# Performance work log

Hardware: AMD Instinct MI355X
Metric: run time of the kernel (lower is better)

Reference implementation:

```python
import jax, jax.numpy as jnp
import numpy as np

IN_CH = 8      # in_channels
CIN = 80       # cin_channels (mel)
DI_BASE = 2
POS_GROUP = 4
NCH = 256      # n_channels
NLAYERS = 8
K = 3          # kernel_size
B = 1          # spect batch; audio batch = B * POS_GROUP
T = 4096
C2L = 2 * NCH * NLAYERS


def _conv1x1(x, w, b):
    # x: [B, C, T], w: [O, C], b: [O]
    return jnp.einsum('bct,oc->bot', x, w) + b[None, :, None]


def _dilated_conv(x, w, b, dilation):
    # x: [B, C, T], w: [O, C, K], 'same' padding as in torch Conv1d
    pad = dilation * (K - 1) // 2
    y = jax.lax.conv_general_dilated(
        x, w, window_strides=(1,), padding=[(pad, pad)],
        rhs_dilation=(dilation,), dimension_numbers=('NCH', 'OIH', 'NCH'))
    return y + b[None, :, None]


def setup_inputs() -> dict:
    key = jax.random.key(0)
    ks = jax.random.split(key, 12)
    s = 0.05
    d = {}
    d['audio'] = jax.random.normal(ks[0], (B * POS_GROUP, IN_CH, T), jnp.float32)
    d['spect'] = jax.random.normal(ks[1], (B, CIN, T), jnp.float32)
    d['pos'] = jax.random.randint(ks[2], (B * POS_GROUP,), 0, POS_GROUP)
    d['start_w'] = jax.random.normal(ks[3], (NCH, IN_CH), jnp.float32) * s
    d['start_b'] = jnp.zeros((NCH,), jnp.float32)
    d['cond_w'] = jax.random.normal(ks[4], (C2L, CIN), jnp.float32) * s
    d['cond_b'] = jnp.zeros((C2L,), jnp.float32)
    d['pos_emb_w'] = jax.random.normal(ks[5], (POS_GROUP, 128), jnp.float32) * s
    d['pos_lin_w'] = jax.random.normal(ks[6], (C2L, 128), jnp.float32) * s
    d['pos_lin_b'] = jnp.zeros((C2L,), jnp.float32)
    d['in_w'] = jax.random.normal(ks[7], (NLAYERS, 2 * NCH, NCH, K), jnp.float32) * s
    d['in_b'] = jnp.zeros((NLAYERS, 2 * NCH), jnp.float32)
    d['rs_w'] = jax.random.normal(ks[8], (NLAYERS - 1, 2 * NCH, NCH), jnp.float32) * s
    d['rs_b'] = jnp.zeros((NLAYERS - 1, 2 * NCH), jnp.float32)
    d['rs_last_w'] = jax.random.normal(ks[9], (NCH, NCH), jnp.float32) * s
    d['rs_last_b'] = jnp.zeros((NCH,), jnp.float32)
    d['end_w'] = jax.random.normal(ks[10], (2 * IN_CH, NCH), jnp.float32) * s
    d['end_b'] = jnp.zeros((2 * IN_CH,), jnp.float32)
    return d


def reference(audio, spect, pos, start_w, start_b, cond_w, cond_b,
              pos_emb_w, pos_lin_w, pos_lin_b, in_w, in_b,
              rs_w, rs_b, rs_last_w, rs_last_b, end_w, end_b):
    h = _conv1x1(audio, start_w, start_b)               # [BG, NCH, T]
    out = jnp.zeros_like(h)
    cond = _conv1x1(spect, cond_w, cond_b)              # [B, 2*NCH*L, T]
    # repeat(1, pos_group, 1).view(-1, C, T) == consecutive batch tiling
    cond = jnp.repeat(cond, POS_GROUP, axis=0)          # [BG, 2*NCH*L, T]
    pe = jax.nn.relu(pos_emb_w[pos])                    # [BG, 128]
    pc = (pe @ pos_lin_w.T + pos_lin_b)[:, :, None]     # [BG, 2*NCH*L, 1]
    for i in range(NLAYERS):
        off = i * 2 * NCH
        in_act = (_dilated_conv(h, in_w[i], in_b[i], DI_BASE ** i)
                  + cond[:, off:off + 2 * NCH]
                  + pc[:, off:off + 2 * NCH])
        acts = jnp.tanh(in_act[:, :NCH]) * jax.nn.sigmoid(in_act[:, NCH:])
        if i < NLAYERS - 1:
            rs = _conv1x1(acts, rs_w[i], rs_b[i])       # [BG, 2*NCH, T]
            h = h + rs[:, :NCH]
            out = out + rs[:, NCH:]
        else:
            out = out + _conv1x1(acts, rs_last_w, rs_last_b)
    y = _conv1x1(out, end_w, end_b)                     # [BG, 2*IN_CH, T]
    return y[:, :IN_CH], y[:, IN_CH:]
```

## Files before the change

### kernel.cpp

```cpp
#include <hip/hip_runtime.h>
#include <stdint.h>

#define T_LEN 4096
#define PAD   128
#define HROWS (T_LEN + 2*PAD)
#define NCH   256
#define M2    512
#define BG    4
#define NL    8

using f4  = __attribute__((ext_vector_type(4))) float;
using bh8 = __attribute__((ext_vector_type(8))) short;
using s4v = __attribute__((ext_vector_type(4))) short;
using u4  = __attribute__((ext_vector_type(4))) unsigned int;

static __device__ __forceinline__ short f2b(float f){
  unsigned u = __builtin_bit_cast(unsigned, f);
  unsigned r = (u + 0x7FFFu + ((u >> 16) & 1u)) >> 16;
  return (short)r;
}
static __device__ __forceinline__ float b2f(short s){
  unsigned u = ((unsigned)(unsigned short)s) << 16;
  return __builtin_bit_cast(float, u);
}

#define MFMA(a,b,c) __builtin_amdgcn_mfma_f32_16x16x32_bf16((a),(b),(c),0,0,0)

#define W_BLK0   0
#define PAD_BLK0 1024
#define E_BLK0   1280
#define ST_BLK0  1408
#define CB_BLK0  1536
#define H0_BLK0  1600
#define ALL_BLKS 1856

__global__ __launch_bounds__(256) void prep_all(
    const float* __restrict__ audio, const float* __restrict__ spect,
    const int* __restrict__ pos, const float* __restrict__ start_w,
    const float* __restrict__ start_b, const float* __restrict__ cond_w,
    const float* __restrict__ pos_emb_w, const float* __restrict__ pos_lin_w,
    const float* __restrict__ pos_lin_b, const float* __restrict__ in_w,
    const float* __restrict__ in_b, const float* __restrict__ rs_w,
    const float* __restrict__ rs_b, const float* __restrict__ rs_last_w,
    const float* __restrict__ rs_last_b, const float* __restrict__ end_w,
    const float* __restrict__ end_b,
    short* __restrict__ W1, short* __restrict__ W2, float* __restrict__ rsb8,
    short* __restrict__ Wc, short* __restrict__ hA, short* __restrict__ hB,
    short* __restrict__ Es, float* __restrict__ ebl, short* __restrict__ spectT,
    float* __restrict__ cb){
  __shared__ float smem[4224];
  const int bid = blockIdx.x, tid = threadIdx.x;

  if (bid < PAD_BLK0){
    const int n1 = NL*3*M2*NCH, n2 = NL*4*8*4*64*8, n3 = NL*M2, n4 = 4096*128;
    for (int i = bid*256 + tid; i < n1+n2+n3+n4; i += 1024*256){
      if (i < n1){
        int j = i & 7, lane = (i >> 3) & 63, mf = (i >> 9) & 3, kk = (i >> 11) & 7, og = (i >> 14) & 7;
        int lt = i >> 17;
        int tap = lt % 3, l = lt / 3;
        int o = og*64 + mf*16 + (lane & 15);
        int c = kk*32 + (lane >> 4)*8 + j;
        W1[i] = f2b(in_w[(((l*M2 + o)*NCH + c)*3) + tap]);
      } else if (i < n1+n2){
        int q = i - n1;
        int j = q & 7, lane = (q >> 3) & 63, mf = (q >> 9) & 3, kk = (q >> 11) & 7, og = (q >> 14) & 3;
        int l = q >> 16;
        int o = og*64 + mf*16 + (lane & 15);
        int c = kk*32 + (lane >> 4)*8 + j;
        W2[q] = (l < 7) ? f2b(rs_w[((size_t)(l*M2 + o))*NCH + c]) : (short)0;
      } else if (i < n1+n2+n3){
        int k = i - n1 - n2;
        int o = k & 511, l = k >> 9;
        rsb8[k] = (l < 7) ? rs_b[l*M2 + o] : 0.f;
      } else {
        int j = i - n1 - n2 - n3;
        int k = j & 127, o = j >> 7;
        Wc[j] = (k < 80) ? f2b(cond_w[o*80 + k]) : (short)0;
      }
    }
  } else if (bid < E_BLK0){
    int i = (bid - PAD_BLK0)*256 + tid;
    short* h = (i < 32768) ? hA : hB;
    int j = (i & 32767) << 3;
    int b = j >> 16;
    int r = j & 65535;
    int row = r >> 8, c = r & 255;
    int grow = (row < PAD) ? row : (T_LEN + PAD + (row - PAD));
    *(u4*)(h + ((size_t)b*HROWS + grow)*NCH + c) = (u4){0,0,0,0};
  } else if (bid < ST_BLK0){
    float* ew_s = smem; float* red = smem + 256;
    int e = bid - E_BLK0;
    const int l = e >> 4, o = e & 15;
    const int c = tid;
    ew_s[c] = end_w[o*256 + c];
    __syncthreads();
    const float* Wsrc = (l < 7) ? (rs_w + ((size_t)(l*M2 + NCH))*NCH) : rs_last_w;
    float acc = 0.f;
    #pragma unroll 8
    for (int cp = 0; cp < 256; ++cp)
      acc += ew_s[cp] * Wsrc[(size_t)cp*NCH + c];
    int kk = c >> 5, g = (c >> 3) & 3, j = c & 7;
    Es[(((size_t)l*8 + kk)*64 + g*16 + o)*8 + j] = f2b(acc);
    float bv = (l < 7) ? rs_b[l*M2 + NCH + c] : rs_last_b[c];
    red[c] = ew_s[c] * bv;
    __syncthreads();
    for (int s = 128; s > 0; s >>= 1){
      if (c < s) red[c] += red[c + s];
      __syncthreads();
    }
    if (c == 0) ebl[l*16 + o] = red[0] + ((l == 0) ? end_b[o] : 0.f);
  } else if (bid < CB_BLK0){
    float (*tile)[65] = (float(*)[65])smem;
    int e = bid - ST_BLK0;
    int t0 = (e & 63)*64, k0 = (e >> 6)*64;
    for (int i = tid; i < 64*64; i += 256){
      int kr = i >> 6, tt = i & 63;
      int k = k0 + kr;
      tile[kr][tt] = (k < 80) ? spect[(size_t)k*T_LEN + t0 + tt] : 0.f;
    }
    __syncthreads();
    for (int i = tid; i < 64*64; i += 256){
      int r = i >> 6, kk = i & 63;
      spectT[(size_t)(t0 + r)*128 + k0 + kk] = f2b(tile[kk][r]);
    }
  } else if (bid < H0_BLK0){
    int e = bid - CB_BLK0;
    int b = e >> 4;
    int ch = (e & 15)*256 + tid;
    int p = pos[b];
    float acc = pos_lin_b[ch] + in_b[ch];
    for (int k = 0; k < 128; ++k){
      float ev = pos_emb_w[p*128 + k];
      ev = ev > 0.f ? ev : 0.f;
      acc += ev * pos_lin_w[ch*128 + k];
    }
    cb[b*4096 + ch] = acc;
  } else {
    float* sw = smem; float* sb = smem + 2048;
    int e = bid - H0_BLK0;
    int b = e >> 6, t0 = (e & 63)*64;
    for (int i = tid; i < NCH*8; i += 256) sw[i] = start_w[i];
    for (int i = tid; i < NCH;   i += 256) sb[i] = start_b[i];
    __syncthreads();
    int t = t0 + (tid & 63);
    int cg = tid >> 6;
    float av[8];
    #pragma unroll
    for (int ic = 0; ic < 8; ++ic) av[ic] = audio[((size_t)(b*8 + ic))*T_LEN + t];
    short* dst = hA + ((size_t)b*HROWS + PAD + t)*NCH;
    for (int c = cg*64; c < cg*64 + 64; ++c){
      float acc = sb[c];
      #pragma unroll
      for (int ic = 0; ic < 8; ++ic) acc += sw[c*8 + ic]*av[ic];
      dst[c] = f2b(acc);
    }
  }
}

__global__ __launch_bounds__(512, 2) void cond_gemm(
    const short* __restrict__ Wc, const short* __restrict__ spectT,
    const float* __restrict__ cond_b, short* __restrict__ cond){
  __shared__ short St[64*128];
  const int tid = threadIdx.x;
  const int w = tid >> 6, lane = tid & 63;
  const int l15 = lane & 15, g = lane >> 4;
  const int t0 = blockIdx.x*64, ch0 = blockIdx.y*512;
  const int orow = w << 6;

  #pragma unroll
  for (int s = 0; s < 2; ++s){
    int id = tid + s*512;
    int r = id >> 4, c8 = (id & 15) << 3;
    u4 v = *(const u4*)(spectT + (size_t)(t0 + r)*128 + c8);
    *(u4*)(St + r*128 + (c8 ^ ((r & 7) << 3))) = v;
  }
  __syncthreads();

  f4 acc[4][4];
  #pragma unroll
  for (int mf = 0; mf < 4; ++mf)
    #pragma unroll
    for (int nf = 0; nf < 4; ++nf) acc[mf][nf] = (f4){0.f,0.f,0.f,0.f};

  #pragma unroll
  for (int kk = 0; kk < 3; ++kk){
    bh8 av[4], bv[4];
    #pragma unroll
    for (int mf = 0; mf < 4; ++mf)
      av[mf] = *(const bh8*)(Wc + (size_t)(ch0 + orow + mf*16 + l15)*128 + kk*32 + g*8);
    #pragma unroll
    for (int nf = 0; nf < 4; ++nf){
      int t = nf*16 + l15;
      bv[nf] = *(const bh8*)(St + t*128 + ((kk*32 + g*8) ^ ((t & 7) << 3)));
    }
    #pragma unroll
    for (int mf = 0; mf < 4; ++mf)
      #pragma unroll
      for (int nf = 0; nf < 4; ++nf)
        acc[mf][nf] = MFMA(av[mf], bv[nf], acc[mf][nf]);
  }

  short* cbase = cond + (((size_t)(blockIdx.y*64 + blockIdx.x)*8 + w)*16)*256 + lane*4;
  #pragma unroll
  for (int mf = 0; mf < 4; ++mf){
    f4 bb = *(const f4*)(cond_b + ch0 + orow + mf*16 + 4*g);
    #pragma unroll
    for (int nf = 0; nf < 4; ++nf){
      s4v pk;
      #pragma unroll
      for (int j = 0; j < 4; ++j) pk[j] = f2b(acc[mf][nf][j] + bb[j]);
      *(s4v*)(cbase + (mf*4 + nf)*256) = pk;
    }
  }
}

__global__ __launch_bounds__(512, 2) void wn_layer(
    const short* __restrict__ hSrc, short* __restrict__ hDst,
    const short* __restrict__ W1l, const short* __restrict__ W2l,
    const short* __restrict__ Esl, const short* __restrict__ condl,
    const float* __restrict__ cb_l, const float* __restrict__ rsb_l,
    const float* __restrict__ ebl_l, float* __restrict__ yacc,
    int dil, int flags){

  __shared__ short Ht[3*64*NCH];
  __shared__ short xb[64*NCH];

  const int tid  = threadIdx.x;
  const int w    = tid >> 6, lane = tid & 63;
  const int l15  = lane & 15, g = lane >> 4;
  const int tile = blockIdx.x, b = blockIdx.y;
  const int orow = w << 6;
  const int sw8  = (l15 & 7) << 3;
  const bool first = flags & 1, last = flags & 2;

  f4 acc[4][4];
  #pragma unroll
  for (int mf = 0; mf < 4; ++mf)
    #pragma unroll
    for (int nf = 0; nf < 4; ++nf) acc[mf][nf] = (f4){0.f,0.f,0.f,0.f};

  bh8 Ap[3][4], Bp[3][4];

#define LA1(S, BUF) do{ const int _tap=(S)>>3, _kk=(S)&7; \
    const short* _p = W1l + (_tap<<17) + (w<<14) + (_kk<<11) + lane*8; \
    Ap[BUF][0]=*(const bh8*)(_p);      Ap[BUF][1]=*(const bh8*)(_p+512); \
    Ap[BUF][2]=*(const bh8*)(_p+1024); Ap[BUF][3]=*(const bh8*)(_p+1536); }while(0)
#define LB1(S, BUF) do{ const int _tap=(S)>>3, _kk=(S)&7; const int _c=(_kk*32+g*8)^sw8; \
    Bp[BUF][0]=*(const bh8*)(Ht + _tap*16384 + ( 0+l15)*NCH + _c); \
    Bp[BUF][1]=*(const bh8*)(Ht + _tap*16384 + (16+l15)*NCH + _c); \
    Bp[BUF][2]=*(const bh8*)(Ht + _tap*16384 + (32+l15)*NCH + _c); \
    Bp[BUF][3]=*(const bh8*)(Ht + _tap*16384 + (48+l15)*NCH + _c); }while(0)
#define LA2(S, BUF) do{ const int _kk=(S); \
    const short* _p = W2l + (w<<14) + (_kk<<11) + lane*8; \
    Ap[BUF][0]=*(const bh8*)(_p);      Ap[BUF][1]=*(const bh8*)(_p+512); \
    Ap[BUF][2]=*(const bh8*)(_p+1024); Ap[BUF][3]=*(const bh8*)(_p+1536); }while(0)
#define LB2(S, BUF) do{ const int _c=((S)*32+g*8)^sw8; \
    Bp[BUF][0]=*(const bh8*)(xb + ( 0+l15)*NCH + _c); \
    Bp[BUF][1]=*(const bh8*)(xb + (16+l15)*NCH + _c); \
    Bp[BUF][2]=*(const bh8*)(xb + (32+l15)*NCH + _c); \
    Bp[BUF][3]=*(const bh8*)(xb + (48+l15)*NCH + _c); }while(0)

  LA1(0, 0);

  {
    const int rsub = tid >> 5;
    const int innr = (tid & 31) << 3;
    #pragma unroll
    for (int tap = 0; tap < 3; ++tap){
      const int gbase = b*HROWS + PAD + tile*64 + (tap-1)*dil;
      #pragma unroll
      for (int ch = 0; ch < 4; ++ch){
        int r = ch*16 + rsub;
        u4 v = *(const u4*)(hSrc + (size_t)(gbase + r)*NCH + innr);
        *(u4*)(Ht + tap*16384 + r*NCH + (innr ^ ((r & 7) << 3))) = v;
      }
    }
  }
  s4v cvf[4][4];
  {
    const short* cbase = condl + (((size_t)tile*8 + w)*16)*256 + lane*4;
    #pragma unroll
    for (int mf = 0; mf < 4; ++mf)
      #pragma unroll
      for (int nf = 0; nf < 4; ++nf)
        cvf[mf][nf] = *(const s4v*)(cbase + (mf*4 + nf)*256);
  }
  __syncthreads();

  LB1(0, 0);
  LA1(1, 1); LB1(1, 1);
  #pragma unroll
  for (int s = 0; s < 24; ++s){
    const int cur = s % 3, pf = (s+2) % 3;
    if (s < 22){ LA1(s+2, pf); LB1(s+2, pf); }
    #pragma unroll
    for (int mf = 0; mf < 4; ++mf)
      #pragma unroll
      for (int nf = 0; nf < 4; ++nf)
        acc[mf][nf] = MFMA(Ap[cur][mf], Bp[cur][nf], acc[mf][nf]);
  }

  float bias[4][4];
  #pragma unroll
  for (int mf = 0; mf < 4; ++mf){
    f4 t = *(const f4*)(cb_l + b*4096 + orow + mf*16 + 4*g);
    #pragma unroll
    for (int j = 0; j < 4; ++j) bias[mf][j] = t[j];
  }
  float rbv[4][4];
  #pragma unroll
  for (int mf = 0; mf < 4; ++mf){
    f4 t = *(const f4*)(rsb_l + orow + mf*16 + 4*g);
    #pragma unroll
    for (int j = 0; j < 4; ++j) rbv[mf][j] = t[j];
  }

  if (w >= 4){
    #pragma unroll
    for (int mf = 0; mf < 4; ++mf){
      #pragma unroll
      for (int nf = 0; nf < 4; ++nf){
        int tl = nf*16 + l15;
        s4v pk;
        #pragma unroll
        for (int j = 0; j < 4; ++j){
          float x = acc[mf][nf][j] + bias[mf][j] + b2f(cvf[mf][nf][j]);
          x = fminf(fmaxf(x, -30.f), 30.f);
          pk[j] = f2b(1.f/(1.f + __expf(-x)));
        }
        int cb0 = (orow - NCH) + mf*16 + 4*g;
        *(s4v*)(xb + tl*NCH + (cb0 ^ sw8)) = pk;
      }
    }
  }
  __syncthreads();
  if (w < 4){
    #pragma unroll
    for (int mf = 0; mf < 4; ++mf){
      #pragma unroll
      for (int nf = 0; nf < 4; ++nf){
        int tl = nf*16 + l15;
        int cb0 = orow + mf*16 + 4*g;
        short* p = xb + tl*NCH + (cb0 ^ sw8);
        s4v sg = *(const s4v*)p;
        s4v pk;
        #pragma unroll
        for (int j = 0; j < 4; ++j){
          float x = acc[mf][nf][j] + bias[mf][j] + b2f(cvf[mf][nf][j]);
          x = fminf(fmaxf(x, -30.f), 30.f);
          float e = __expf(2.f*x);
          float th = (e - 1.f)/(e + 1.f);
          pk[j] = f2b(th * b2f(sg[j]));
        }
        *(s4v*)p = pk;
      }
    }
    if (!last) LA2(0, 0);
  }
  __syncthreads();

  if (w < 4){
    if (!last){
      #pragma unroll
      for (int mf = 0; mf < 4; ++mf)
        #pragma unroll
        for (int nf = 0; nf < 4; ++nf) acc[mf][nf] = (f4){0.f,0.f,0.f,0.f};
      LB2(0, 0);
      #pragma unroll
      for (int s = 0; s < 8; ++s){
        const int cur = s & 1, nxt = cur ^ 1;
        if (s < 7){ LA2(s+1, nxt); LB2(s+1, nxt); }
        #pragma unroll
        for (int mf = 0; mf < 4; ++mf)
          #pragma unroll
          for (int nf = 0; nf < 4; ++nf)
            acc[mf][nf] = MFMA(Ap[cur][mf], Bp[cur][nf], acc[mf][nf]);
      }
      #pragma unroll
      for (int mf = 0; mf < 4; ++mf){
        #pragma unroll
        for (int nf = 0; nf < 4; ++nf){
          int tl = nf*16 + l15;
          int cb0 = orow + mf*16 + 4*g;
          s4v hold = *(const s4v*)(Ht + 16384 + tl*NCH + (cb0 ^ sw8));
          s4v pk;
          #pragma unroll
          for (int j = 0; j < 4; ++j)
            pk[j] = f2b(b2f(hold[j]) + acc[mf][nf][j] + rbv[mf][j]);
          *(s4v*)(hDst + ((size_t)b*HROWS + PAD + tile*64 + tl)*NCH + cb0) = pk;
        }
      }
    }
  } else {
    const int q = w - 4;
    f4 ya = (f4){0.f,0.f,0.f,0.f};
    #pragma unroll
    for (int kk = 0; kk < 8; ++kk){
      bh8 av = *(const bh8*)(Esl + ((size_t)kk*64 + lane)*8);
      int _c = (kk*32 + g*8) ^ sw8;
      bh8 bv = *(const bh8*)(xb + (q*16 + l15)*NCH + _c);
      ya = MFMA(av, bv, ya);
    }
    float* yp = yacc + ((size_t)b*T_LEN + tile*64 + q*16 + l15)*16 + g*4;
    f4 prev = first ? (f4){0.f,0.f,0.f,0.f} : *(const f4*)yp;
    f4 o;
    #pragma unroll
    for (int j = 0; j < 4; ++j) o[j] = prev[j] + ya[j] + ebl_l[g*4 + j];
    *(f4*)yp = o;
  }
#undef LA1
#undef LB1
#undef LA2
#undef LB2
}

__global__ void final_y(const float* __restrict__ yacc, float* __restrict__ y){
  __shared__ float tl[16][65];
  int b = blockIdx.y, t0 = blockIdx.x*64;
  int i = threadIdx.x;
  #pragma unroll
  for (int s = 0; s < 4; ++s){
    int idx = i + s*256;
    int t = idx >> 4, o = idx & 15;
    tl[o][t] = yacc[((size_t)b*T_LEN + t0 + t)*16 + o];
  }
  __syncthreads();
  #pragma unroll
  for (int s = 0; s < 4; ++s){
    int idx = i + s*256;
    int o = idx >> 6, t = idx & 63;
    float v = tl[o][t];
    float* dst = (o < 8) ? (y + ((size_t)(b*8 + o))*T_LEN)
                         : (y + 131072 + ((size_t)(b*8 + o - 8))*T_LEN);
    dst[t0 + t] = v;
  }
}

extern "C" void kernel_launch(void* const* d_in, const int* in_sizes, int n_in,
                              void* d_out, int out_size, void* d_ws, size_t ws_size,
                              hipStream_t stream){
  const float* audio      = (const float*)d_in[0];
  const float* spect      = (const float*)d_in[1];
  const int*   pos        = (const int*)  d_in[2];
  const float* start_w    = (const float*)d_in[3];
  const float* start_b    = (const float*)d_in[4];
  const float* cond_w     = (const float*)d_in[5];
  const float* cond_b     = (const float*)d_in[6];
  const float* pos_emb_w  = (const float*)d_in[7];
  const float* pos_lin_w  = (const float*)d_in[8];
  const float* pos_lin_b  = (const float*)d_in[9];
  const float* in_w       = (const float*)d_in[10];
  const float* in_b       = (const float*)d_in[11];
  const float* rs_w       = (const float*)d_in[12];
  const float* rs_b       = (const float*)d_in[13];
  const float* rs_last_w  = (const float*)d_in[14];
  const float* rs_last_b  = (const float*)d_in[15];
  const float* end_w      = (const float*)d_in[16];
  const float* end_b      = (const float*)d_in[17];
  float* y = (float*)d_out;

  char* ws = (char*)d_ws;
  size_t off = 0;
  auto alloc = [&](size_t bytes) -> void* {
    void* p = ws + off;
    off += (bytes + 255) & ~(size_t)255;
    return p;
  };
  const size_t hBytes   = (size_t)BG*HROWS*NCH*2;
  const size_t condBy   = (size_t)4096*T_LEN*2;
  short* hA     = (short*)alloc(hBytes);
  short* hB     = (short*)alloc(hBytes);
  short* cond   = (short*)alloc(condBy);
  short* W1     = (short*)alloc((size_t)NL*3*M2*NCH*2);
  short* W2     = (short*)alloc((size_t)NL*4*16384*2);
  float* rsb8   = (float*)alloc((size_t)NL*M2*4);
  float* cb     = (float*)alloc((size_t)BG*4096*4);
  short* Wc     = (short*)alloc((size_t)4096*128*2);
  short* spectT = (short*)alloc((size_t)4096*128*2);
  short* Es     = (short*)alloc((size_t)NL*8*64*8*2);
  float* ebl    = (float*)alloc((size_t)NL*16*4);
  float* yacc   = (float*)alloc((size_t)BG*T_LEN*16*4);
  if (off > ws_size) return;

  prep_all<<<ALL_BLKS, 256, 0, stream>>>(
      audio, spect, pos, start_w, start_b, cond_w, pos_emb_w, pos_lin_w,
      pos_lin_b, in_w, in_b, rs_w, rs_b, rs_last_w, rs_last_b, end_w, end_b,
      W1, W2, rsb8, Wc, hA, hB, Es, ebl, spectT, cb);

  cond_gemm<<<dim3(64, 8), 512, 0, stream>>>(Wc, spectT, cond_b, cond);

  for (int l = 0; l < NL; ++l){
    const short* hS = (l & 1) ? hB : hA;
    short*       hD = (l & 1) ? hA : hB;
    int flags = (l == 0 ? 1 : 0) | (l == NL-1 ? 2 : 0);
    wn_layer<<<dim3(64, BG), 512, 0, stream>>>(
        hS, hD,
        W1 + (size_t)l*3*M2*NCH,
        W2 + (size_t)l*4*16384,
        Es + (size_t)l*8*64*8,
        cond + (size_t)l*64*8*16*256,
        cb + l*M2,
        rsb8 + l*M2,
        ebl + l*16,
        yacc, 1 << l, flags);
  }
  final_y<<<dim3(64, BG), 256, 0, stream>>>(yacc, y);
}
```

Before: 273.1 us.

## Fuse conditioning GEMM into WaveNet layer and interleave gate channels per wave

Removes the separate cond_gemm kernel and its large bf16 cond buffer. Each layer now computes the conditioning projection from the spectrogram as three extra K-steps in the same MFMA accumulators, with cond_b folded into the per-channel bias. Weights are re-laid out so each wave holds both the tanh and sigmoid halves of 32 channels, which computes the gated activation in registers without an extra LDS round trip and barrier. All 8 waves now share the residual GEMM and the end projection, the latter split into two K halves that are summed in final_y. This trades a 64 MB cond write and read for redundant cond compute across the 4 batches and extra LDS for the spectrogram tile.

```diff
diff --git a/kernel.cpp b/kernel.cpp
--- a/kernel.cpp
+++ b/kernel.cpp
@@ -26,7 +26,7 @@
 
 #define MFMA(a,b,c) __builtin_amdgcn_mfma_f32_16x16x32_bf16((a),(b),(c),0,0,0)
 
-#define W_BLK0   0
+
 #define PAD_BLK0 1024
 #define E_BLK0   1280
 #define ST_BLK0  1408
@@ -38,44 +38,50 @@
     const float* __restrict__ audio, const float* __restrict__ spect,
     const int* __restrict__ pos, const float* __restrict__ start_w,
     const float* __restrict__ start_b, const float* __restrict__ cond_w,
-    const float* __restrict__ pos_emb_w, const float* __restrict__ pos_lin_w,
-    const float* __restrict__ pos_lin_b, const float* __restrict__ in_w,
-    const float* __restrict__ in_b, const float* __restrict__ rs_w,
-    const float* __restrict__ rs_b, const float* __restrict__ rs_last_w,
-    const float* __restrict__ rs_last_b, const float* __restrict__ end_w,
-    const float* __restrict__ end_b,
-    short* __restrict__ W1, short* __restrict__ W2, float* __restrict__ rsb8,
-    short* __restrict__ Wc, short* __restrict__ hA, short* __restrict__ hB,
+    const float* __restrict__ cond_b, const float* __restrict__ pos_emb_w,
+    const float* __restrict__ pos_lin_w, const float* __restrict__ pos_lin_b,
+    const float* __restrict__ in_w, const float* __restrict__ in_b,
+    const float* __restrict__ rs_w, const float* __restrict__ rs_b,
+    const float* __restrict__ rs_last_w, const float* __restrict__ rs_last_b,
+    const float* __restrict__ end_w, const float* __restrict__ end_b,
+    short* __restrict__ W1, short* __restrict__ W2, short* __restrict__ Wcn,
+    float* __restrict__ rsb8, short* __restrict__ hA, short* __restrict__ hB,
     short* __restrict__ Es, float* __restrict__ ebl, short* __restrict__ spectT,
     float* __restrict__ cb){
   __shared__ float smem[4224];
   const int bid = blockIdx.x, tid = threadIdx.x;
 
   if (bid < PAD_BLK0){
-    const int n1 = NL*3*M2*NCH, n2 = NL*4*8*4*64*8, n3 = NL*M2, n4 = 4096*128;
-    for (int i = bid*256 + tid; i < n1+n2+n3+n4; i += 1024*256){
+    const int n1 = NL*3*8*8*4*512;
+    const int n2 = NL*8*8*2*512;
+    const int n4 = NL*8*4*4*512;
+    const int n3 = NL*M2;
+    for (int i = bid*256 + tid; i < n1+n2+n4+n3; i += 1024*256){
       if (i < n1){
-        int j = i & 7, lane = (i >> 3) & 63, mf = (i >> 9) & 3, kk = (i >> 11) & 7, og = (i >> 14) & 7;
+        int j = i & 7, lane = (i >> 3) & 63, f = (i >> 9) & 3, kk = (i >> 11) & 7, w = (i >> 14) & 7;
         int lt = i >> 17;
         int tap = lt % 3, l = lt / 3;
-        int o = og*64 + mf*16 + (lane & 15);
+        int o = (f < 2) ? (w*32 + f*16 + (lane & 15)) : (256 + w*32 + (f-2)*16 + (lane & 15));
         int c = kk*32 + (lane >> 4)*8 + j;
         W1[i] = f2b(in_w[(((l*M2 + o)*NCH + c)*3) + tap]);
       } else if (i < n1+n2){
         int q = i - n1;
-        int j = q & 7, lane = (q >> 3) & 63, mf = (q >> 9) & 3, kk = (q >> 11) & 7, og = (q >> 14) & 3;
+        int j = q & 7, lane = (q >> 3) & 63, f = (q >> 9) & 1, kk = (q >> 10) & 7, w = (q >> 13) & 7;
         int l = q >> 16;
-        int o = og*64 + mf*16 + (lane & 15);
+        int o = w*32 + f*16 + (lane & 15);
         int c = kk*32 + (lane >> 4)*8 + j;
         W2[q] = (l < 7) ? f2b(rs_w[((size_t)(l*M2 + o))*NCH + c]) : (short)0;
-      } else if (i < n1+n2+n3){
-        int k = i - n1 - n2;
+      } else if (i < n1+n2+n4){
+        int r = i - n1 - n2;
+        int j = r & 7, lane = (r >> 3) & 63, f = (r >> 9) & 3, kk = (r >> 11) & 3, w = (r >> 13) & 7;
+        int l = r >> 16;
+        int o = (f < 2) ? (w*32 + f*16 + (lane & 15)) : (256 + w*32 + (f-2)*16 + (lane & 15));
+        int k = kk*32 + (lane >> 4)*8 + j;
+        Wcn[r] = (k < 80) ? f2b(cond_w[(size_t)(l*M2 + o)*80 + k]) : (short)0;
+      } else {
+        int k = i - n1 - n2 - n4;
         int o = k & 511, l = k >> 9;
         rsb8[k] = (l < 7) ? rs_b[l*M2 + o] : 0.f;
-      } else {
-        int j = i - n1 - n2 - n3;
-        int k = j & 127, o = j >> 7;
-        Wc[j] = (k < 80) ? f2b(cond_w[o*80 + k]) : (short)0;
       }
     }
   } else if (bid < E_BLK0){
@@ -128,7 +134,7 @@
     int b = e >> 4;
     int ch = (e & 15)*256 + tid;
     int p = pos[b];
-    float acc = pos_lin_b[ch] + in_b[ch];
+    float acc = pos_lin_b[ch] + in_b[ch] + cond_b[ch];
     for (int k = 0; k < 128; ++k){
       float ev = pos_emb_w[p*128 + k];
       ev = ev > 0.f ? ev : 0.f;
@@ -157,92 +163,44 @@
   }
 }
 
-__global__ __launch_bounds__(512, 2) void cond_gemm(
-    const short* __restrict__ Wc, const short* __restrict__ spectT,
-    const float* __restrict__ cond_b, short* __restrict__ cond){
-  __shared__ short St[64*128];
-  const int tid = threadIdx.x;
-  const int w = tid >> 6, lane = tid & 63;
-  const int l15 = lane & 15, g = lane >> 4;
-  const int t0 = blockIdx.x*64, ch0 = blockIdx.y*512;
-  const int orow = w << 6;
-
-  #pragma unroll
-  for (int s = 0; s < 2; ++s){
-    int id = tid + s*512;
-    int r = id >> 4, c8 = (id & 15) << 3;
-    u4 v = *(const u4*)(spectT + (size_t)(t0 + r)*128 + c8);
-    *(u4*)(St + r*128 + (c8 ^ ((r & 7) << 3))) = v;
-  }
-  __syncthreads();
-
-  f4 acc[4][4];
-  #pragma unroll
-  for (int mf = 0; mf < 4; ++mf)
-    #pragma unroll
-    for (int nf = 0; nf < 4; ++nf) acc[mf][nf] = (f4){0.f,0.f,0.f,0.f};
-
-  #pragma unroll
-  for (int kk = 0; kk < 3; ++kk){
-    bh8 av[4], bv[4];
-    #pragma unroll
-    for (int mf = 0; mf < 4; ++mf)
-      av[mf] = *(const bh8*)(Wc + (size_t)(ch0 + orow + mf*16 + l15)*128 + kk*32 + g*8);
-    #pragma unroll
-    for (int nf = 0; nf < 4; ++nf){
-      int t = nf*16 + l15;
-      bv[nf] = *(const bh8*)(St + t*128 + ((kk*32 + g*8) ^ ((t & 7) << 3)));
-    }
-    #pragma unroll
-    for (int mf = 0; mf < 4; ++mf)
-      #pragma unroll
-      for (int nf = 0; nf < 4; ++nf)
-        acc[mf][nf] = MFMA(av[mf], bv[nf], acc[mf][nf]);
-  }
-
-  short* cbase = cond + (((size_t)(blockIdx.y*64 + blockIdx.x)*8 + w)*16)*256 + lane*4;
-  #pragma unroll
-  for (int mf = 0; mf < 4; ++mf){
-    f4 bb = *(const f4*)(cond_b + ch0 + orow + mf*16 + 4*g);
-    #pragma unroll
-    for (int nf = 0; nf < 4; ++nf){
-      s4v pk;
-      #pragma unroll
-      for (int j = 0; j < 4; ++j) pk[j] = f2b(acc[mf][nf][j] + bb[j]);
-      *(s4v*)(cbase + (mf*4 + nf)*256) = pk;
-    }
-  }
-}
-
 __global__ __launch_bounds__(512, 2) void wn_layer(
     const short* __restrict__ hSrc, short* __restrict__ hDst,
     const short* __restrict__ W1l, const short* __restrict__ W2l,
-    const short* __restrict__ Esl, const short* __restrict__ condl,
+    const short* __restrict__ Wcl, const short* __restrict__ Esl,
+    const short* __restrict__ spectTp,
     const float* __restrict__ cb_l, const float* __restrict__ rsb_l,
     const float* __restrict__ ebl_l, float* __restrict__ yacc,
     int dil, int flags){
 
   __shared__ short Ht[3*64*NCH];
   __shared__ short xb[64*NCH];
+  __shared__ short St[64*128];
 
   const int tid  = threadIdx.x;
   const int w    = tid >> 6, lane = tid & 63;
   const int l15  = lane & 15, g = lane >> 4;
   const int tile = blockIdx.x, b = blockIdx.y;
-  const int orow = w << 6;
   const int sw8  = (l15 & 7) << 3;
   const bool first = flags & 1, last = flags & 2;
 
   f4 acc[4][4];
   #pragma unroll
-  for (int mf = 0; mf < 4; ++mf)
-    #pragma unroll
-    for (int nf = 0; nf < 4; ++nf) acc[mf][nf] = (f4){0.f,0.f,0.f,0.f};
+  for (int f = 0; f < 4; ++f)
+    #pragma unroll
+    for (int nf = 0; nf < 4; ++nf) acc[f][nf] = (f4){0.f,0.f,0.f,0.f};
 
   bh8 Ap[3][4], Bp[3][4];
 
+#define LAc(S, BUF) do{ const short* _p = Wcl + w*8192 + (S)*2048 + lane*8; \
+    Ap[BUF][0]=*(const bh8*)(_p);      Ap[BUF][1]=*(const bh8*)(_p+512); \
+    Ap[BUF][2]=*(const bh8*)(_p+1024); Ap[BUF][3]=*(const bh8*)(_p+1536); }while(0)
+#define LBc(S, BUF) do{ const int _c=((S)*32+g*8)^sw8; \
+    Bp[BUF][0]=*(const bh8*)(St + ( 0+l15)*128 + _c); \
+    Bp[BUF][1]=*(const bh8*)(St + (16+l15)*128 + _c); \
+    Bp[BUF][2]=*(const bh8*)(St + (32+l15)*128 + _c); \
+    Bp[BUF][3]=*(const bh8*)(St + (48+l15)*128 + _c); }while(0)
 #define LA1(S, BUF) do{ const int _tap=(S)>>3, _kk=(S)&7; \
-    const short* _p = W1l + (_tap<<17) + (w<<14) + (_kk<<11) + lane*8; \
+    const short* _p = W1l + _tap*131072 + w*16384 + _kk*2048 + lane*8; \
     Ap[BUF][0]=*(const bh8*)(_p);      Ap[BUF][1]=*(const bh8*)(_p+512); \
     Ap[BUF][2]=*(const bh8*)(_p+1024); Ap[BUF][3]=*(const bh8*)(_p+1536); }while(0)
 #define LB1(S, BUF) do{ const int _tap=(S)>>3, _kk=(S)&7; const int _c=(_kk*32+g*8)^sw8; \
@@ -250,17 +208,18 @@
     Bp[BUF][1]=*(const bh8*)(Ht + _tap*16384 + (16+l15)*NCH + _c); \
     Bp[BUF][2]=*(const bh8*)(Ht + _tap*16384 + (32+l15)*NCH + _c); \
     Bp[BUF][3]=*(const bh8*)(Ht + _tap*16384 + (48+l15)*NCH + _c); }while(0)
-#define LA2(S, BUF) do{ const int _kk=(S); \
-    const short* _p = W2l + (w<<14) + (_kk<<11) + lane*8; \
-    Ap[BUF][0]=*(const bh8*)(_p);      Ap[BUF][1]=*(const bh8*)(_p+512); \
-    Ap[BUF][2]=*(const bh8*)(_p+1024); Ap[BUF][3]=*(const bh8*)(_p+1536); }while(0)
+#define LAX(S, BUF) do{ if((S)<3) LAc((S),BUF); else LA1((S)-3,BUF); }while(0)
+#define LBX(S, BUF) do{ if((S)<3) LBc((S),BUF); else LB1((S)-3,BUF); }while(0)
+#define LA2(S, BUF) do{ \
+    const short* _p = W2l + w*8192 + (S)*1024 + lane*8; \
+    Ap[BUF][0]=*(const bh8*)(_p);      Ap[BUF][1]=*(const bh8*)(_p+512); }while(0)
 #define LB2(S, BUF) do{ const int _c=((S)*32+g*8)^sw8; \
     Bp[BUF][0]=*(const bh8*)(xb + ( 0+l15)*NCH + _c); \
     Bp[BUF][1]=*(const bh8*)(xb + (16+l15)*NCH + _c); \
     Bp[BUF][2]=*(const bh8*)(xb + (32+l15)*NCH + _c); \
     Bp[BUF][3]=*(const bh8*)(xb + (48+l15)*NCH + _c); }while(0)
 
-  LA1(0, 0);
+  LAX(0, 0);
 
   {
     const int rsub = tid >> 5;
@@ -275,141 +234,123 @@
         *(u4*)(Ht + tap*16384 + r*NCH + (innr ^ ((r & 7) << 3))) = v;
       }
     }
-  }
-  s4v cvf[4][4];
-  {
-    const short* cbase = condl + (((size_t)tile*8 + w)*16)*256 + lane*4;
-    #pragma unroll
-    for (int mf = 0; mf < 4; ++mf)
+    #pragma unroll
+    for (int s = 0; s < 2; ++s){
+      int id = tid + s*512;
+      int r = id >> 4, c8 = (id & 15) << 3;
+      u4 v = *(const u4*)(spectTp + (size_t)(tile*64 + r)*128 + c8);
+      *(u4*)(St + r*128 + (c8 ^ ((r & 7) << 3))) = v;
+    }
+  }
+  __syncthreads();
+
+  LBX(0, 0);
+  LAX(1, 1); LBX(1, 1);
+  #pragma unroll
+  for (int s = 0; s < 27; ++s){
+    const int cur = s % 3, pf = (s+2) % 3;
+    if (s < 25){ LAX(s+2, pf); LBX(s+2, pf); }
+    #pragma unroll
+    for (int f = 0; f < 4; ++f)
       #pragma unroll
       for (int nf = 0; nf < 4; ++nf)
-        cvf[mf][nf] = *(const s4v*)(cbase + (mf*4 + nf)*256);
-  }
+        acc[f][nf] = MFMA(Ap[cur][f], Bp[cur][nf], acc[f][nf]);
+  }
+
+  float bias[4][4];
+  #pragma unroll
+  for (int f = 0; f < 4; ++f){
+    int ch = ((f < 2) ? (w*32 + f*16) : (256 + w*32 + (f-2)*16)) + 4*g;
+    f4 t = *(const f4*)(cb_l + b*4096 + ch);
+    #pragma unroll
+    for (int j = 0; j < 4; ++j) bias[f][j] = t[j];
+  }
+  float rbv[2][4];
+  #pragma unroll
+  for (int f = 0; f < 2; ++f){
+    f4 t = *(const f4*)(rsb_l + w*32 + f*16 + 4*g);
+    #pragma unroll
+    for (int j = 0; j < 4; ++j) rbv[f][j] = t[j];
+  }
+
+  #pragma unroll
+  for (int f = 0; f < 2; ++f){
+    #pragma unroll
+    for (int nf = 0; nf < 4; ++nf){
+      int tl = nf*16 + l15;
+      s4v pk;
+      #pragma unroll
+      for (int j = 0; j < 4; ++j){
+        float xl = acc[f][nf][j]   + bias[f][j];
+        float xh = acc[f+2][nf][j] + bias[f+2][j];
+        xl = fminf(fmaxf(xl, -30.f), 30.f);
+        xh = fminf(fmaxf(xh, -30.f), 30.f);
+        float e2 = __expf(2.f*xl);
+        float th = (e2 - 1.f)/(e2 + 1.f);
+        float sg = 1.f/(1.f + __expf(-xh));
+        pk[j] = f2b(th * sg);
+      }
+      *(s4v*)(xb + tl*NCH + ((w*32 + f*16 + 4*g) ^ sw8)) = pk;
+    }
+  }
+  if (!last) LA2(0, 0);
   __syncthreads();
 
-  LB1(0, 0);
-  LA1(1, 1); LB1(1, 1);
-  #pragma unroll
-  for (int s = 0; s < 24; ++s){
-    const int cur = s % 3, pf = (s+2) % 3;
-    if (s < 22){ LA1(s+2, pf); LB1(s+2, pf); }
-    #pragma unroll
-    for (int mf = 0; mf < 4; ++mf)
-      #pragma unroll
-      for (int nf = 0; nf < 4; ++nf)
-        acc[mf][nf] = MFMA(Ap[cur][mf], Bp[cur][nf], acc[mf][nf]);
-  }
-
-  float bias[4][4];
-  #pragma unroll
-  for (int mf = 0; mf < 4; ++mf){
-    f4 t = *(const f4*)(cb_l + b*4096 + orow + mf*16 + 4*g);
-    #pragma unroll
-    for (int j = 0; j < 4; ++j) bias[mf][j] = t[j];
-  }
-  float rbv[4][4];
-  #pragma unroll
-  for (int mf = 0; mf < 4; ++mf){
-    f4 t = *(const f4*)(rsb_l + orow + mf*16 + 4*g);
-    #pragma unroll
-    for (int j = 0; j < 4; ++j) rbv[mf][j] = t[j];
-  }
-
-  if (w >= 4){
-    #pragma unroll
-    for (int mf = 0; mf < 4; ++mf){
+  if (!last){
+    #pragma unroll
+    for (int f = 0; f < 2; ++f)
+      #pragma unroll
+      for (int nf = 0; nf < 4; ++nf) acc[f][nf] = (f4){0.f,0.f,0.f,0.f};
+    LB2(0, 0);
+    #pragma unroll
+    for (int s = 0; s < 8; ++s){
+      const int cur = s & 1, nxt = cur ^ 1;
+      if (s < 7){ LA2(s+1, nxt); LB2(s+1, nxt); }
+      #pragma unroll
+      for (int f = 0; f < 2; ++f)
+        #pragma unroll
+        for (int nf = 0; nf < 4; ++nf)
+          acc[f][nf] = MFMA(Ap[cur][f], Bp[cur][nf], acc[f][nf]);
+    }
+    #pragma unroll
+    for (int f = 0; f < 2; ++f){
       #pragma unroll
       for (int nf = 0; nf < 4; ++nf){
         int tl = nf*16 + l15;
+        int cb0 = w*32 + f*16 + 4*g;
+        s4v hold = *(const s4v*)(Ht + 16384 + tl*NCH + (cb0 ^ sw8));
         s4v pk;
         #pragma unroll
-        for (int j = 0; j < 4; ++j){
-          float x = acc[mf][nf][j] + bias[mf][j] + b2f(cvf[mf][nf][j]);
-          x = fminf(fmaxf(x, -30.f), 30.f);
-          pk[j] = f2b(1.f/(1.f + __expf(-x)));
-        }
-        int cb0 = (orow - NCH) + mf*16 + 4*g;
-        *(s4v*)(xb + tl*NCH + (cb0 ^ sw8)) = pk;
+        for (int j = 0; j < 4; ++j)
+          pk[j] = f2b(b2f(hold[j]) + acc[f][nf][j] + rbv[f][j]);
+        *(s4v*)(hDst + ((size_t)b*HROWS + PAD + tile*64 + tl)*NCH + cb0) = pk;
       }
     }
   }
-  __syncthreads();
-  if (w < 4){
-    #pragma unroll
-    for (int mf = 0; mf < 4; ++mf){
-      #pragma unroll
-      for (int nf = 0; nf < 4; ++nf){
-        int tl = nf*16 + l15;
-        int cb0 = orow + mf*16 + 4*g;
-        short* p = xb + tl*NCH + (cb0 ^ sw8);
-        s4v sg = *(const s4v*)p;
-        s4v pk;
-        #pragma unroll
-        for (int j = 0; j < 4; ++j){
-          float x = acc[mf][nf][j] + bias[mf][j] + b2f(cvf[mf][nf][j]);
-          x = fminf(fmaxf(x, -30.f), 30.f);
-          float e = __expf(2.f*x);
-          float th = (e - 1.f)/(e + 1.f);
-          pk[j] = f2b(th * b2f(sg[j]));
-        }
-        *(s4v*)p = pk;
-      }
-    }
-    if (!last) LA2(0, 0);
-  }
-  __syncthreads();
-
-  if (w < 4){
-    if (!last){
-      #pragma unroll
-      for (int mf = 0; mf < 4; ++mf)
-        #pragma unroll
-        for (int nf = 0; nf < 4; ++nf) acc[mf][nf] = (f4){0.f,0.f,0.f,0.f};
-      LB2(0, 0);
-      #pragma unroll
-      for (int s = 0; s < 8; ++s){
-        const int cur = s & 1, nxt = cur ^ 1;
-        if (s < 7){ LA2(s+1, nxt); LB2(s+1, nxt); }
-        #pragma unroll
-        for (int mf = 0; mf < 4; ++mf)
-          #pragma unroll
-          for (int nf = 0; nf < 4; ++nf)
-            acc[mf][nf] = MFMA(Ap[cur][mf], Bp[cur][nf], acc[mf][nf]);
-      }
-      #pragma unroll
-      for (int mf = 0; mf < 4; ++mf){
-        #pragma unroll
-        for (int nf = 0; nf < 4; ++nf){
-          int tl = nf*16 + l15;
-          int cb0 = orow + mf*16 + 4*g;
-          s4v hold = *(const s4v*)(Ht + 16384 + tl*NCH + (cb0 ^ sw8));
-          s4v pk;
-          #pragma unroll
-          for (int j = 0; j < 4; ++j)
-            pk[j] = f2b(b2f(hold[j]) + acc[mf][nf][j] + rbv[mf][j]);
-          *(s4v*)(hDst + ((size_t)b*HROWS + PAD + tile*64 + tl)*NCH + cb0) = pk;
-        }
-      }
-    }
-  } else {
-    const int q = w - 4;
+  {
+    const int nfq = w & 3, kh = w >> 2;
     f4 ya = (f4){0.f,0.f,0.f,0.f};
     #pragma unroll
-    for (int kk = 0; kk < 8; ++kk){
-      bh8 av = *(const bh8*)(Esl + ((size_t)kk*64 + lane)*8);
-      int _c = (kk*32 + g*8) ^ sw8;
-      bh8 bv = *(const bh8*)(xb + (q*16 + l15)*NCH + _c);
+    for (int s = 0; s < 4; ++s){
+      int kks = kh*4 + s;
+      bh8 av = *(const bh8*)(Esl + ((size_t)kks*64 + lane)*8);
+      bh8 bv = *(const bh8*)(xb + (nfq*16 + l15)*NCH + ((kks*32 + g*8) ^ sw8));
       ya = MFMA(av, bv, ya);
     }
-    float* yp = yacc + ((size_t)b*T_LEN + tile*64 + q*16 + l15)*16 + g*4;
+    float* yp = yacc + (((size_t)(b*T_LEN + tile*64 + nfq*16 + l15))*2 + kh)*16 + g*4;
     f4 prev = first ? (f4){0.f,0.f,0.f,0.f} : *(const f4*)yp;
     f4 o;
     #pragma unroll
-    for (int j = 0; j < 4; ++j) o[j] = prev[j] + ya[j] + ebl_l[g*4 + j];
+    for (int j = 0; j < 4; ++j)
+      o[j] = prev[j] + ya[j] + ((kh == 0) ? ebl_l[g*4 + j] : 0.f);
     *(f4*)yp = o;
   }
+#undef LAc
+#undef LBc
 #undef LA1
 #undef LB1
+#undef LAX
+#undef LBX
 #undef LA2
 #undef LB2
 }
@@ -422,7 +363,8 @@
   for (int s = 0; s < 4; ++s){
     int idx = i + s*256;
     int t = idx >> 4, o = idx & 15;
-    tl[o][t] = yacc[((size_t)b*T_LEN + t0 + t)*16 + o];
+    size_t base = ((size_t)(b*T_LEN + t0 + t))*32 + o;
+    tl[o][t] = yacc[base] + yacc[base + 16];
   }
   __syncthreads();
   #pragma unroll
@@ -466,28 +408,24 @@
     off += (bytes + 255) & ~(size_t)255;
     return p;
   };
-  const size_t hBytes   = (size_t)BG*HROWS*NCH*2;
-  const size_t condBy   = (size_t)4096*T_LEN*2;
+  const size_t hBytes = (size_t)BG*HROWS*NCH*2;
   short* hA     = (short*)alloc(hBytes);
   short* hB     = (short*)alloc(hBytes);
-  short* cond   = (short*)alloc(condBy);
-  short* W1     = (short*)alloc((size_t)NL*3*M2*NCH*2);
-  short* W2     = (short*)alloc((size_t)NL*4*16384*2);
+  short* W1     = (short*)alloc((size_t)NL*3*8*8*4*512*2);
+  short* W2     = (short*)alloc((size_t)NL*8*8*2*512*2);
+  short* Wcn    = (short*)alloc((size_t)NL*8*4*4*512*2);
   float* rsb8   = (float*)alloc((size_t)NL*M2*4);
   float* cb     = (float*)alloc((size_t)BG*4096*4);
-  short* Wc     = (short*)alloc((size_t)4096*128*2);
   short* spectT = (short*)alloc((size_t)4096*128*2);
   short* Es     = (short*)alloc((size_t)NL*8*64*8*2);
   float* ebl    = (float*)alloc((size_t)NL*16*4);
-  float* yacc   = (float*)alloc((size_t)BG*T_LEN*16*4);
+  float* yacc   = (float*)alloc((size_t)BG*T_LEN*2*16*4);
   if (off > ws_size) return;
 
   prep_all<<<ALL_BLKS, 256, 0, stream>>>(
-      audio, spect, pos, start_w, start_b, cond_w, pos_emb_w, pos_lin_w,
+      audio, spect, pos, start_w, start_b, cond_w, cond_b, pos_emb_w, pos_lin_w,
       pos_lin_b, in_w, in_b, rs_w, rs_b, rs_last_w, rs_last_b, end_w, end_b,
-      W1, W2, rsb8, Wc, hA, hB, Es, ebl, spectT, cb);
-
-  cond_gemm<<<dim3(64, 8), 512, 0, stream>>>(Wc, spectT, cond_b, cond);
+      W1, W2, Wcn, rsb8, hA, hB, Es, ebl, spectT, cb);
 
   for (int l = 0; l < NL; ++l){
     const short* hS = (l & 1) ? hB : hA;
@@ -495,10 +433,11 @@
     int flags = (l == 0 ? 1 : 0) | (l == NL-1 ? 2 : 0);
     wn_layer<<<dim3(64, BG), 512, 0, stream>>>(
         hS, hD,
-        W1 + (size_t)l*3*M2*NCH,
-        W2 + (size_t)l*4*16384,
-        Es + (size_t)l*8*64*8,
-        cond + (size_t)l*64*8*16*256,
+        W1 + (size_t)l*3*131072,
+        W2 + (size_t)l*65536,
+        Wcn + (size_t)l*65536,
+        Es + (size_t)l*4096,
+        spectT,
         cb + l*M2,
         rsb8 + l*M2,
         ebl + l*16,
```

New measurement: 219.6 us. 1.24x faster.
